# Kernel optimization log

Hardware: AMD Instinct MI355X
Metric: run time of the kernel (lower is better)

The kernel has to match this reference:

```python
import jax, jax.numpy as jnp
import numpy as np

B, S, D_IN, D_OUT, NUM_LAYERS = 128, 64, 2048, 2048, 64

def setup_inputs() -> dict:
    key = jax.random.key(0)
    k1, k2, k3 = jax.random.split(key, 3)
    x = jax.random.normal(k1, (B, S, D_IN), dtype=jnp.float32)
    weight = jax.random.normal(k2, (NUM_LAYERS, D_OUT, D_IN), dtype=jnp.float32)
    layer_idx = jax.random.randint(k3, (S,), 0, NUM_LAYERS, dtype=jnp.int32)
    return {"x": x, "weight": weight, "layer_idx": layer_idx}

def reference(x, weight, layer_idx):
    # x: [B, S, D_in]; weight: [L, D_out, D_in]; layer_idx: [S] ints in [0, L)
    # Per position s: out[:, s, :] = x[:, s, :] @ weight[layer_idx[s]].T
    w_sel = weight[layer_idx]                      # [S, D_out, D_in] gather
    out = jnp.einsum('bsd,sod->bso', x, w_sel)     # batched per-position GEMMs
    return out
```

## Files before the change

### kernel.cpp

```cpp
#include <hip/hip_runtime.h>
#include <hip/hip_bf16.h>

#define B_DIM 128
#define S_DIM 64
#define DIN   2048
#define DOUT  2048
#define NLAYERS 64

#define BM 128
#define BN 64
#define BK 64
#define NK (DIN / BK)
#define TPP (DOUT / BN)
#define NTILES (S_DIM * TPP)
#define NXCD 8
#define APAD 16384

typedef __bf16 bf16_t;
typedef __attribute__((ext_vector_type(8))) bf16_t bf16x8;
typedef __attribute__((ext_vector_type(4))) float f32x4;

__global__ void rank_sort(const int* __restrict__ layer_idx, int* __restrict__ perm) {
    __shared__ int L[S_DIM];
    const int s = threadIdx.x;
    L[s] = layer_idx[s];
    __syncthreads();
    const int mine = L[s];
    int rank = 0;
    #pragma unroll
    for (int t = 0; t < S_DIM; ++t) {
        const int lt = L[t];
        rank += (lt < mine || (lt == mine && t < s)) ? 1 : 0;
    }
    perm[rank] = s;
}

__global__ void convert_x(const float* __restrict__ x, bf16_t* __restrict__ x16) {
    const size_t i = ((size_t)blockIdx.x * 256 + threadIdx.x) * 8;
    f32x4 a = *(const f32x4*)(x + i);
    f32x4 b = *(const f32x4*)(x + i + 4);
    bf16x8 v;
    #pragma unroll
    for (int j = 0; j < 4; ++j) { v[j] = (bf16_t)a[j]; v[j + 4] = (bf16_t)b[j]; }
    *(bf16x8*)(x16 + i) = v;
}

template <bool XBF16>
__launch_bounds__(256, 2)
__global__ void flex_linear_gemm(const float* __restrict__ x,
                                 const bf16_t* __restrict__ x16,
                                 const float* __restrict__ w,
                                 const int* __restrict__ layer_idx,
                                 const int* __restrict__ perm,
                                 float* __restrict__ out) {
    __shared__ bf16_t Alds[BM * BK + APAD];
    __shared__ bf16_t Blds[BN * BK];

    const int orig = blockIdx.x;
    const int xcd  = orig & (NXCD - 1);
    const int slot = orig >> 3;
    const int tile = xcd * (NTILES / NXCD) + slot;
    const int yy   = tile / TPP;
    const int nb   = tile % TPP;

    const int s  = perm[yy];
    const int layer = layer_idx[s];

    const float* Bg = w + (size_t)layer * (size_t)(DOUT * DIN) + (size_t)(nb * BN) * DIN;

    const int tid  = threadIdx.x;
    const int lane = tid & 63;
    const int wave = tid >> 6;
    const int wr = (wave >> 1) * 64;
    const int wc = (wave & 1) * 32;
    const int lrow = lane & 15;
    const int lk   = (lane >> 4) * 8;

    int offWA[4], offWB[2];
    const float*  pA[4];
    const bf16_t* pA16[4];
    const float*  pB[2];
    #pragma unroll
    for (int i = 0; i < 4; ++i) {
        const int c   = tid + 256 * i;
        const int row = c >> 3;
        const int kc8 = (c & 7) * 8;
        offWA[i] = (row * BK + kc8) ^ ((row & 7) << 3);
        const size_t aoff = (size_t)row * (S_DIM * DIN) + (size_t)s * DIN + kc8;
        pA[i]   = x   + aoff;
        pA16[i] = x16 + aoff;
    }
    #pragma unroll
    for (int i = 0; i < 2; ++i) {
        const int c   = tid + 256 * i;
        const int row = c >> 3;
        const int kc8 = (c & 7) * 8;
        offWB[i] = (row * BK + kc8) ^ ((row & 7) << 3);
        pB[i] = Bg + (size_t)row * DIN + kc8;
    }
    int offA[2][4], offB[2][2];
    #pragma unroll
    for (int kk = 0; kk < 2; ++kk) {
        #pragma unroll
        for (int m = 0; m < 4; ++m) {
            const int ra = wr + m * 16 + lrow;
            offA[kk][m] = (ra * BK + kk * 32 + lk) ^ ((ra & 7) << 3);
        }
        #pragma unroll
        for (int n = 0; n < 2; ++n) {
            const int rb = wc + n * 16 + lrow;
            offB[kk][n] = (rb * BK + kk * 32 + lk) ^ ((rb & 7) << 3);
        }
    }

    bf16x8 RA16[4];
    f32x4  RA[8];
    f32x4  RB[4];
    f32x4  acc[4][2] = {};

    auto issue = [&](int kb) {
        const int koff = kb * BK;
        #pragma unroll
        for (int i = 0; i < 4; ++i) {
            if constexpr (XBF16) {
                RA16[i] = *(const bf16x8*)(pA16[i] + koff);
            } else {
                const float* a = pA[i] + koff;
                RA[2 * i]     = *(const f32x4*)a;
                RA[2 * i + 1] = *(const f32x4*)(a + 4);
            }
        }
        #pragma unroll
        for (int i = 0; i < 2; ++i) {
            const float* b = pB[i] + koff;
            RB[2 * i]     = *(const f32x4*)b;
            RB[2 * i + 1] = *(const f32x4*)(b + 4);
        }
    };
    auto cvt_write = [&]() {
        #pragma unroll
        for (int i = 0; i < 4; ++i) {
            if constexpr (XBF16) {
                *(bf16x8*)&Alds[offWA[i]] = RA16[i];
            } else {
                bf16x8 va;
                #pragma unroll
                for (int j = 0; j < 4; ++j) {
                    va[j]     = (bf16_t)RA[2 * i][j];
                    va[j + 4] = (bf16_t)RA[2 * i + 1][j];
                }
                *(bf16x8*)&Alds[offWA[i]] = va;
            }
        }
        #pragma unroll
        for (int i = 0; i < 2; ++i) {
            bf16x8 vb;
            #pragma unroll
            for (int j = 0; j < 4; ++j) {
                vb[j]     = (bf16_t)RB[2 * i][j];
                vb[j + 4] = (bf16_t)RB[2 * i + 1][j];
            }
            *(bf16x8*)&Blds[offWB[i]] = vb;
        }
    };
    auto compute = [&]() {
        #pragma unroll
        for (int kk = 0; kk < 2; ++kk) {
            bf16x8 af[4], bfr[2];
            #pragma unroll
            for (int m = 0; m < 4; ++m) af[m]  = *(const bf16x8*)&Alds[offA[kk][m]];
            #pragma unroll
            for (int n = 0; n < 2; ++n) bfr[n] = *(const bf16x8*)&Blds[offB[kk][n]];
            #pragma unroll
            for (int m = 0; m < 4; ++m)
                #pragma unroll
                for (int n = 0; n < 2; ++n)
                    acc[m][n] = __builtin_amdgcn_mfma_f32_16x16x32_bf16(af[m], bfr[n], acc[m][n], 0, 0, 0);
        }
    };

    issue(0);
    cvt_write();
    for (int kb = 0; kb < NK - 1; ++kb) {
        __syncthreads();
        issue(kb + 1);
        compute();
        __syncthreads();
        cvt_write();
    }
    __syncthreads();
    compute();

    float* Og = out + (size_t)s * DOUT + (size_t)(nb * BN);
    #pragma unroll
    for (int m = 0; m < 4; ++m) {
        const int rb = wr + m * 16 + (lane >> 4) * 4;
        #pragma unroll
        for (int r = 0; r < 4; ++r) {
            float* orow = Og + (size_t)(rb + r) * (S_DIM * DOUT);
            #pragma unroll
            for (int n = 0; n < 2; ++n)
                __builtin_nontemporal_store(acc[m][n][r], &orow[wc + n * 16 + (lane & 15)]);
        }
    }
}

extern "C" void kernel_launch(void* const* d_in, const int* in_sizes, int n_in,
                              void* d_out, int out_size, void* d_ws, size_t ws_size,
                              hipStream_t stream) {
    const float* x         = (const float*)d_in[0];
    const float* w         = (const float*)d_in[1];
    const int*   layer_idx = (const int*)d_in[2];
    float*       out       = (float*)d_out;

    int*    perm = (int*)d_ws;
    bf16_t* x16  = (bf16_t*)((char*)d_ws + 512);
    const size_t need = 512 + (size_t)B_DIM * S_DIM * DIN * sizeof(bf16_t);

    rank_sort<<<1, S_DIM, 0, stream>>>(layer_idx, perm);

    if (ws_size >= need) {
        convert_x<<<(B_DIM * S_DIM * DIN / 8) / 256, 256, 0, stream>>>(x, x16);
        flex_linear_gemm<true><<<NTILES, dim3(256), 0, stream>>>(x, x16, w, layer_idx, perm, out);
    } else {
        flex_linear_gemm<false><<<NTILES, dim3(256), 0, stream>>>(x, x16, w, layer_idx, perm, out);
    }
}
```

Baseline: 228.6 us.

## Double-buffer LDS tiles to drop one barrier per K iteration

Splits the A and B shared-memory tiles into two ping-pong buffers. Each iteration computes on one buffer while converting and storing the next tile into the other, so only one __syncthreads per K step is needed instead of two. Global loads are now issued two tiles ahead, after the conversion. The A padding is cut from 16384 to 2048 elements per buffer so total LDS stays roughly the same and two blocks per CU can still fit.

```diff
diff --git a/kernel.cpp b/kernel.cpp
--- a/kernel.cpp
+++ b/kernel.cpp
@@ -14,7 +14,7 @@
 #define TPP (DOUT / BN)
 #define NTILES (S_DIM * TPP)
 #define NXCD 8
-#define APAD 16384
+#define APADE 2048
 
 typedef __bf16 bf16_t;
 typedef __attribute__((ext_vector_type(8))) bf16_t bf16x8;
@@ -53,8 +53,8 @@
                                  const int* __restrict__ layer_idx,
                                  const int* __restrict__ perm,
                                  float* __restrict__ out) {
-    __shared__ bf16_t Alds[BM * BK + APAD];
-    __shared__ bf16_t Blds[BN * BK];
+    __shared__ bf16_t Alds[2][BM * BK + APADE];
+    __shared__ bf16_t Blds[2][BN * BK];
 
     const int orig = blockIdx.x;
     const int xcd  = orig & (NXCD - 1);
@@ -137,11 +137,13 @@
             RB[2 * i + 1] = *(const f32x4*)(b + 4);
         }
     };
-    auto cvt_write = [&]() {
+    auto cvt_write = [&](int buf) {
+        bf16_t* Al = &Alds[buf][0];
+        bf16_t* Bl = &Blds[buf][0];
         #pragma unroll
         for (int i = 0; i < 4; ++i) {
             if constexpr (XBF16) {
-                *(bf16x8*)&Alds[offWA[i]] = RA16[i];
+                *(bf16x8*)&Al[offWA[i]] = RA16[i];
             } else {
                 bf16x8 va;
                 #pragma unroll
@@ -149,7 +151,7 @@
                     va[j]     = (bf16_t)RA[2 * i][j];
                     va[j + 4] = (bf16_t)RA[2 * i + 1][j];
                 }
-                *(bf16x8*)&Alds[offWA[i]] = va;
+                *(bf16x8*)&Al[offWA[i]] = va;
             }
         }
         #pragma unroll
@@ -160,17 +162,19 @@
                 vb[j]     = (bf16_t)RB[2 * i][j];
                 vb[j + 4] = (bf16_t)RB[2 * i + 1][j];
             }
-            *(bf16x8*)&Blds[offWB[i]] = vb;
+            *(bf16x8*)&Bl[offWB[i]] = vb;
         }
     };
-    auto compute = [&]() {
+    auto compute = [&](int buf) {
+        const bf16_t* Al = &Alds[buf][0];
+        const bf16_t* Bl = &Blds[buf][0];
         #pragma unroll
         for (int kk = 0; kk < 2; ++kk) {
             bf16x8 af[4], bfr[2];
             #pragma unroll
-            for (int m = 0; m < 4; ++m) af[m]  = *(const bf16x8*)&Alds[offA[kk][m]];
-            #pragma unroll
-            for (int n = 0; n < 2; ++n) bfr[n] = *(const bf16x8*)&Blds[offB[kk][n]];
+            for (int m = 0; m < 4; ++m) af[m]  = *(const bf16x8*)&Al[offA[kk][m]];
+            #pragma unroll
+            for (int n = 0; n < 2; ++n) bfr[n] = *(const bf16x8*)&Bl[offB[kk][n]];
             #pragma unroll
             for (int m = 0; m < 4; ++m)
                 #pragma unroll
@@ -180,16 +184,16 @@
     };
 
     issue(0);
-    cvt_write();
+    cvt_write(0);
+    issue(1);
     for (int kb = 0; kb < NK - 1; ++kb) {
         __syncthreads();
-        issue(kb + 1);
-        compute();
-        __syncthreads();
-        cvt_write();
+        compute(kb & 1);
+        cvt_write((kb + 1) & 1);
+        if (kb + 2 < NK) issue(kb + 2);
     }
     __syncthreads();
-    compute();
+    compute((NK - 1) & 1);
 
     float* Og = out + (size_t)s * DOUT + (size_t)(nb * BN);
     #pragma unroll
```

Result: no change. 231.8 us (+1.4%).
